# Performance work log

Hardware: AMD Instinct MI355X
Metric: run time of the kernel (lower is better)

Reference implementation:

```python
import jax, jax.numpy as jnp
import numpy as np

B, N, H, D, HS, RS = 4, 512, 16, 64, 1024, 64  # HS = H*D, HSIZE_INSIDE == HSIZE
SCALE = 1.0 / float(np.sqrt(D))


def setup_inputs() -> dict:
    key = jax.random.key(0)
    ks = jax.random.split(key, 11)
    s = 0.02
    return {
        "v": jax.random.normal(ks[0], (B, N, HS), jnp.float32),
        "k": jax.random.normal(ks[1], (B, N, HS), jnp.float32),
        "q": jax.random.normal(ks[2], (B, N, HS), jnp.float32),
        "mask": jax.random.randint(ks[3], (B, 1, N, N), 0, 2).astype(bool),
        "rel_embed": jax.random.uniform(ks[4], (B, N, N, RS), jnp.float32),
        # weights stored as [in, out] (torch Linear applies x @ W.T)
        "Wv": jax.random.normal(ks[5], (HS, HS), jnp.float32) * s,
        "Wk": jax.random.normal(ks[6], (HS, HS), jnp.float32) * s,
        "Wq": jax.random.normal(ks[7], (HS, HS), jnp.float32) * s,
        "Wr": jax.random.normal(ks[8], (RS, H), jnp.float32) * s,
        "br": jax.random.normal(ks[9], (H,), jnp.float32) * s,
        "Wm": jax.random.normal(ks[10], (HS, HS), jnp.float32) * s,
    }


def reference(v, k, q, mask, rel_embed, Wv, Wk, Wq, Wr, br, Wm):
    b, nq, _ = q.shape

    def proj(x, W):  # [b, n, HS] -> [b, H, n, D]
        return (x @ W).reshape(b, -1, H, D).transpose(0, 2, 1, 3)

    vh, kh, qh = proj(v, Wv), proj(k, Wk), proj(q, Wq)
    # learned relative-position bias: relu -> clamp -> log, [b, H, nq, nk]
    r = jax.nn.relu(rel_embed @ Wr + br)
    bias = jnp.log(jnp.clip(r, 1e-6, None)).transpose(0, 3, 1, 2)
    scores = jnp.einsum('bhqd,bhkd->bhqk', qh, kh) * SCALE + bias
    scores = jnp.where(mask, jnp.float32(-1e9), scores)
    att = jax.nn.softmax(scores, axis=-1)  # dropout_r = 0
    atted = jnp.einsum('bhqk,bhkd->bhqd', att, vh)
    atted = atted.transpose(0, 2, 1, 3).reshape(b, nq, H * D)
    return atted @ Wm
```

## Files before the change

### kernel.cpp

```cpp
#include <hip/hip_runtime.h>
#include <hip/hip_bf16.h>


typedef __bf16 bf16_t;
typedef __bf16 bf16x8 __attribute__((ext_vector_type(8)));
typedef float f32x4 __attribute__((ext_vector_type(4)));

__device__ __forceinline__ f32x4 mfma16(bf16x8 a, bf16x8 b, f32x4 c) {
  return __builtin_amdgcn_mfma_f32_16x16x32_bf16(a, b, c, 0, 0, 0);
}
__device__ __forceinline__ f32x4 zero4() {
  f32x4 z; z[0] = 0.f; z[1] = 0.f; z[2] = 0.f; z[3] = 0.f; return z;
}

#define GLOAD_LDS16(gptr, lptr)                                                   \
  __builtin_amdgcn_global_load_lds(                                               \
      (const __attribute__((address_space(1))) unsigned int*)(gptr),              \
      (__attribute__((address_space(3))) unsigned int*)(lptr), 16, 0, 0)

__global__ __launch_bounds__(256) void wtrans_kernel(
    const float* __restrict__ W0, const float* __restrict__ W1,
    const float* __restrict__ W2, const float* __restrict__ W3,
    bf16_t* __restrict__ OutBase,
    const unsigned int* __restrict__ mw, int* __restrict__ flag) {
  const float* W = blockIdx.z == 0 ? W0 : blockIdx.z == 1 ? W1 : blockIdx.z == 2 ? W2 : W3;
  bf16_t* Ot = OutBase + (size_t)blockIdx.z * 1024 * 1024;
  __shared__ float tile[64][68];
  __shared__ int sflag;
  const int tid = threadIdx.x;
  const bool probe = (blockIdx.x == 0 && blockIdx.y == 0 && blockIdx.z == 0);
  if (probe && tid == 0) sflag = 0;
  const int i0 = blockIdx.y * 64, j0 = blockIdx.x * 64;
  const int ri = tid >> 2, rc = (tid & 3) * 16;
  const float* src = W + (size_t)(i0 + ri) * 1024 + j0 + rc;
#pragma unroll
  for (int qq = 0; qq < 4; ++qq) {
    float4 f = *(const float4*)(src + qq * 4);
    *(float4*)(&tile[ri][rc + qq * 4]) = f;
  }
  if (probe) {
    int any = 0;
    for (int i = tid; i < 4096; i += 256) any |= (mw[i] > 1u) ? 1 : 0;
    if (any) atomicOr(&sflag, 1);
  }
  __syncthreads();
  const int wj = tid >> 2, wc = (tid & 3) * 16;
  bf16x8 o0, o1;
#pragma unroll
  for (int s = 0; s < 8; ++s) o0[s] = (bf16_t)tile[wc + s][wj];
#pragma unroll
  for (int s = 0; s < 8; ++s) o1[s] = (bf16_t)tile[wc + 8 + s][wj];
  bf16_t* dst = Ot + (size_t)(j0 + wj) * 1024 + i0 + wc;
  *(bf16x8*)dst = o0;
  *(bf16x8*)(dst + 8) = o1;
  if (probe && tid == 0) *flag = sflag;
}

__global__ __launch_bounds__(256) void cast_qkv(
    const float* __restrict__ q, const float* __restrict__ k, const float* __restrict__ v,
    bf16_t* __restrict__ Qc, bf16_t* __restrict__ Kc, bf16_t* __restrict__ Vc) {
  const size_t gid = (size_t)blockIdx.x * 256 + threadIdx.x;
  const int which = (int)(gid >> 18);
  const size_t off = (gid & 262143) * 8;
  const float* src = which == 0 ? q : which == 1 ? k : v;
  bf16_t* dst = which == 0 ? Qc : which == 1 ? Kc : Vc;
  const float scl = which == 0 ? 0.125f : 1.0f;
  float4 f0 = *(const float4*)(src + off);
  float4 f1 = *(const float4*)(src + off + 4);
  bf16x8 o;
  o[0] = (bf16_t)(f0.x * scl); o[1] = (bf16_t)(f0.y * scl);
  o[2] = (bf16_t)(f0.z * scl); o[3] = (bf16_t)(f0.w * scl);
  o[4] = (bf16_t)(f1.x * scl); o[5] = (bf16_t)(f1.y * scl);
  o[6] = (bf16_t)(f1.z * scl); o[7] = (bf16_t)(f1.w * scl);
  *(bf16x8*)(dst + off) = o;
}

__global__ __launch_bounds__(256) void proj_gemm2(
    const bf16_t* __restrict__ Aq, const bf16_t* __restrict__ Ak, const bf16_t* __restrict__ Av,
    const bf16_t* __restrict__ Bq, const bf16_t* __restrict__ Bk, const bf16_t* __restrict__ Bv,
    bf16_t* __restrict__ Oq, bf16_t* __restrict__ Ok, bf16_t* __restrict__ Ov) {
  const int z = blockIdx.z;
  const bf16_t* A = (z == 0) ? Aq : (z == 1) ? Ak : Av;
  const bf16_t* Bt = (z == 0) ? Bq : (z == 1) ? Bk : Bv;
  bf16_t* Out = (z == 0) ? Oq : (z == 1) ? Ok : Ov;
  __shared__ __align__(16) bf16_t Asm[128 * 64];
  __shared__ __align__(16) bf16_t Bsm[128 * 64];
  const int tid = threadIdx.x, wid = tid >> 6, lane = tid & 63;
  const int lg = lane >> 4, lc = lane & 15;
  const int m0 = blockIdx.y * 128, n0 = blockIdx.x * 128;
  const int wm = (wid >> 1) * 64, wn = (wid & 1) * 64;
  const int sr = lane >> 3;
  const int scch = lane & 7;
  const int srcch = scch ^ sr;
  const bf16_t* Ap[4];
  const bf16_t* Bp[4];
#pragma unroll
  for (int i = 0; i < 4; ++i) {
    const int r = wid * 32 + i * 8 + sr;
    Ap[i] = A + (size_t)(m0 + r) * 1024 + srcch * 8;
    Bp[i] = Bt + (size_t)(n0 + r) * 1024 + srcch * 8;
  }
  f32x4 acc[4][4];
#pragma unroll
  for (int i = 0; i < 4; ++i)
#pragma unroll
    for (int j = 0; j < 4; ++j) acc[i][j] = zero4();

  for (int k0 = 0; k0 < 1024; k0 += 64) {
#pragma unroll
    for (int i = 0; i < 4; ++i) {
      GLOAD_LDS16(Ap[i] + k0, Asm + (wid * 32 + i * 8) * 64);
      GLOAD_LDS16(Bp[i] + k0, Bsm + (wid * 32 + i * 8) * 64);
    }
    __syncthreads();
#pragma unroll
    for (int kk = 0; kk < 2; ++kk) {
      bf16x8 af[4], bfv[4];
#pragma unroll
      for (int i = 0; i < 4; ++i) {
        const int ar = wm + i * 16 + lc;
        af[i] = *(const bf16x8*)(Asm + ar * 64 + ((kk * 4 + lg) ^ (ar & 7)) * 8);
        const int brr = wn + i * 16 + lc;
        bfv[i] = *(const bf16x8*)(Bsm + brr * 64 + ((kk * 4 + lg) ^ (brr & 7)) * 8);
      }
#pragma unroll
      for (int mi = 0; mi < 4; ++mi)
#pragma unroll
        for (int ni = 0; ni < 4; ++ni) acc[mi][ni] = mfma16(af[mi], bfv[ni], acc[mi][ni]);
    }
    __syncthreads();
  }
#pragma unroll
  for (int mi = 0; mi < 4; ++mi)
#pragma unroll
    for (int ni = 0; ni < 4; ++ni)
#pragma unroll
      for (int j = 0; j < 4; ++j) {
        const int m = m0 + wm + mi * 16 + lg * 4 + j;
        const int col = n0 + wn + ni * 16 + lc;
        const int b = m >> 9, n = m & 511;
        const int h = col >> 6, d = col & 63;
        Out[(((size_t)(b * 16 + h)) * 512 + n) * 64 + d] = (bf16_t)acc[mi][ni][j];
      }
}

__global__ __launch_bounds__(256) void bias_kernel(
    const float* __restrict__ rel, const float* __restrict__ Wr,
    const float* __restrict__ br, const void* __restrict__ mask,
    const int* __restrict__ mflag, bf16_t* __restrict__ biasM) {
  const int tid = threadIdx.x, wid = tid >> 6, lane = tid & 63;
  const int lg = lane >> 4, lc = lane & 15;
  const int pair = blockIdx.x;
  const int b = pair >> 9, qrow = pair & 511;
  const int isU8 = *mflag;
  bf16x8 wf[2];
#pragma unroll
  for (int kk = 0; kk < 2; ++kk)
#pragma unroll
    for (int j = 0; j < 8; ++j)
      wf[kk][j] = (bf16_t)Wr[(kk * 32 + lg * 8 + j) * 16 + lc];
  float brv[4];
#pragma unroll
  for (int j = 0; j < 4; ++j) brv[j] = br[lg * 4 + j];
  const float* relrow = rel + (size_t)pair * 512 * 64;
  const size_t mbase = (size_t)b * 512 * 512 + (size_t)qrow * 512;
  bf16_t* outb = biasM + (size_t)b * 16 * 512 * 512 + (size_t)qrow * 512;
#pragma unroll 4
  for (int kt = wid * 8; kt < wid * 8 + 8; ++kt) {
    const int k0 = kt * 16;
    const float* rrow = relrow + (size_t)(k0 + lc) * 64;
    f32x4 acc;
    acc[0] = brv[0]; acc[1] = brv[1]; acc[2] = brv[2]; acc[3] = brv[3];
#pragma unroll
    for (int kk = 0; kk < 2; ++kk) {
      const float4* s = (const float4*)(rrow + kk * 32 + lg * 8);
      float4 f0 = s[0], f1 = s[1];
      bf16x8 bfr;
      bfr[0] = (bf16_t)f0.x; bfr[1] = (bf16_t)f0.y; bfr[2] = (bf16_t)f0.z; bfr[3] = (bf16_t)f0.w;
      bfr[4] = (bf16_t)f1.x; bfr[5] = (bf16_t)f1.y; bfr[6] = (bf16_t)f1.z; bfr[7] = (bf16_t)f1.w;
      acc = mfma16(wf[kk], bfr, acc);
    }
    bool mb;
    if (isU8) mb = ((const unsigned char*)mask)[mbase + k0 + lc] != 0;
    else      mb = ((const int*)mask)[mbase + k0 + lc] != 0;
#pragma unroll
    for (int j = 0; j < 4; ++j) {
      const float valf = mb ? -1e9f : __logf(fmaxf(acc[j], 1e-6f));
      outb[(size_t)(lg * 4 + j) * 512 * 512 + k0 + lc] = (bf16_t)valf;
    }
  }
}

__global__ __launch_bounds__(256) void attn_kernel(
    const bf16_t* __restrict__ Qh, const bf16_t* __restrict__ Kh,
    const bf16_t* __restrict__ Vh, const bf16_t* __restrict__ biasM,
    bf16_t* __restrict__ atted) {
  __shared__ __align__(16) bf16_t Ksm[2][64 * 64];
  __shared__ __align__(16) bf16_t Vtsm[2][64 * 88];
  __shared__ __align__(16) bf16_t Psm[4 * 16 * 64];
  const int tid = threadIdx.x, wid = tid >> 6, lane = tid & 63;
  const int lg = lane >> 4, lc = lane & 15;
  const int bid = blockIdx.x;
  const int qt = bid & 7, h = (bid >> 3) & 15, b = bid >> 7;
  const size_t headoff = (size_t)(b * 16 + h) * 512 * 64;
  const bf16_t* Qb = Qh + headoff;
  const bf16_t* Kb = Kh + headoff;
  const bf16_t* Vb = Vh + headoff;
  const int q0 = qt * 64 + wid * 16;
  const bf16_t* biasb = biasM + ((size_t)(b * 16 + h) * 512 + q0) * 512;

  bf16x8 qf[2];
#pragma unroll
  for (int kk = 0; kk < 2; ++kk)
    qf[kk] = *(const bf16x8*)(Qb + (size_t)(q0 + lc) * 64 + kk * 32 + lg * 8);

  f32x4 Oacc[4];
#pragma unroll
  for (int ds = 0; ds < 4; ++ds) Oacc[ds] = zero4();
  float mrun[4], lrun[4];
#pragma unroll
  for (int j = 0; j < 4; ++j) { mrun[j] = -INFINITY; lrun[j] = 0.f; }

  const int krow = tid & 63, kc0 = (tid >> 6) * 2;
  const int vn = tid & 63, vd0 = (tid >> 6) * 16;
  bf16_t* Pw = Psm + wid * 16 * 64;

#define STAGE(T, BUF)                                                          \
  do {                                                                         \
    const int kb_ = (T) * 64;                                                  \
    _Pragma("unroll") for (int ci = 0; ci < 2; ++ci) {                         \
      const int c_ = kc0 + ci;                                                 \
      bf16x8 kv_ = *(const bf16x8*)(Kb + (size_t)(kb_ + krow) * 64 + c_ * 8);  \
      *(bf16x8*)(Ksm[BUF] + krow * 64 + (c_ ^ (krow & 7)) * 8) = kv_;          \
    }                                                                          \
    bf16x8 v0_ = *(const bf16x8*)(Vb + (size_t)(kb_ + vn) * 64 + vd0);         \
    bf16x8 v1_ = *(const bf16x8*)(Vb + (size_t)(kb_ + vn) * 64 + vd0 + 8);     \
    _Pragma("unroll") for (int i = 0; i < 8; ++i)                              \
        Vtsm[BUF][(vd0 + i) * 88 + vn] = v0_[i];                               \
    _Pragma("unroll") for (int i = 0; i < 8; ++i)                              \
        Vtsm[BUF][(vd0 + 8 + i) * 88 + vn] = v1_[i];                           \
  } while (0)

  STAGE(0, 0);
  __syncthreads();

  for (int t = 0; t < 8; ++t) {
    const int cur = t & 1;
    if (t < 7) STAGE(t + 1, cur ^ 1);

    f32x4 sacc[4];
#pragma unroll
    for (int quad = 0; quad < 4; ++quad)
#pragma unroll
      for (int j = 0; j < 4; ++j)
        sacc[quad][j] = (float)biasb[(size_t)(lg * 4 + j) * 512 + t * 64 + quad * 16 + lc];

    const bf16_t* Kc = Ksm[cur];
#pragma unroll
    for (int quad = 0; quad < 4; ++quad) {
      const int kr = quad * 16 + lc;
#pragma unroll
      for (int kk = 0; kk < 2; ++kk) {
        bf16x8 kf = *(const bf16x8*)(Kc + kr * 64 + ((kk * 4 + lg) ^ (kr & 7)) * 8);
        sacc[quad] = mfma16(qf[kk], kf, sacc[quad]);
      }
    }

    float p[4][4];
#pragma unroll
    for (int j = 0; j < 4; ++j) {
      float tmax = fmaxf(fmaxf(sacc[0][j], sacc[1][j]), fmaxf(sacc[2][j], sacc[3][j]));
#pragma unroll
      for (int mm = 1; mm < 16; mm <<= 1) tmax = fmaxf(tmax, __shfl_xor(tmax, mm));
      const float mnew = fmaxf(mrun[j], tmax);
      const float sf = __expf(mrun[j] - mnew);
      mrun[j] = mnew;
      lrun[j] *= sf;
#pragma unroll
      for (int ds = 0; ds < 4; ++ds) Oacc[ds][j] *= sf;
      float psum = 0.f;
#pragma unroll
      for (int quad = 0; quad < 4; ++quad) {
        const float pv = __expf(sacc[quad][j] - mnew);
        p[quad][j] = pv;
        psum += pv;
      }
      lrun[j] += psum;
    }

#pragma unroll
    for (int quad = 0; quad < 4; ++quad)
#pragma unroll
      for (int j = 0; j < 4; ++j) {
        const int row = lg * 4 + j, col = quad * 16 + lc;
        Pw[row * 64 + ((col >> 3) ^ (row & 7)) * 8 + (col & 7)] = (bf16_t)p[quad][j];
      }

    const bf16_t* Vc = Vtsm[cur];
#pragma unroll
    for (int kk = 0; kk < 2; ++kk) {
      bf16x8 pf = *(const bf16x8*)(Pw + lc * 64 + ((kk * 4 + lg) ^ (lc & 7)) * 8);
#pragma unroll
      for (int ds = 0; ds < 4; ++ds) {
        bf16x8 vf = *(const bf16x8*)(Vc + (ds * 16 + lc) * 88 + kk * 32 + lg * 8);
        Oacc[ds] = mfma16(pf, vf, Oacc[ds]);
      }
    }
    __syncthreads();
  }
#undef STAGE

#pragma unroll
  for (int j = 0; j < 4; ++j) {
    float l = lrun[j];
#pragma unroll
    for (int mm = 1; mm < 16; mm <<= 1) l += __shfl_xor(l, mm);
    lrun[j] = 1.0f / l;
  }
#pragma unroll
  for (int ds = 0; ds < 4; ++ds)
#pragma unroll
    for (int j = 0; j < 4; ++j) {
      const int n = q0 + lg * 4 + j;
      const int d = ds * 16 + lc;
      atted[((size_t)b * 512 + n) * 1024 + h * 64 + d] = (bf16_t)(Oacc[ds][j] * lrun[j]);
    }
}

__global__ __launch_bounds__(256) void out_gemm2(
    const bf16_t* __restrict__ A, const bf16_t* __restrict__ Bt, float* __restrict__ Out) {
  __shared__ __align__(16) bf16_t Asm[128 * 64];
  __shared__ __align__(16) bf16_t Bsm[128 * 64];
  const int tid = threadIdx.x, wid = tid >> 6, lane = tid & 63;
  const int lg = lane >> 4, lc = lane & 15;
  const int m0 = blockIdx.y * 128, n0 = blockIdx.x * 128;
  const int wm = (wid >> 1) * 64, wn = (wid & 1) * 64;
  const int sr = lane >> 3, scch = lane & 7;
  const int srcch = scch ^ sr;
  const bf16_t* Ap[4];
  const bf16_t* Bp[4];
#pragma unroll
  for (int i = 0; i < 4; ++i) {
    const int r = wid * 32 + i * 8 + sr;
    Ap[i] = A + (size_t)(m0 + r) * 1024 + srcch * 8;
    Bp[i] = Bt + (size_t)(n0 + r) * 1024 + srcch * 8;
  }
  f32x4 acc[4][4];
#pragma unroll
  for (int i = 0; i < 4; ++i)
#pragma unroll
    for (int j = 0; j < 4; ++j) acc[i][j] = zero4();

  for (int k0 = 0; k0 < 1024; k0 += 64) {
#pragma unroll
    for (int i = 0; i < 4; ++i) {
      GLOAD_LDS16(Ap[i] + k0, Asm + (wid * 32 + i * 8) * 64);
      GLOAD_LDS16(Bp[i] + k0, Bsm + (wid * 32 + i * 8) * 64);
    }
    __syncthreads();
#pragma unroll
    for (int kk = 0; kk < 2; ++kk) {
      bf16x8 af[4], bfv[4];
#pragma unroll
      for (int i = 0; i < 4; ++i) {
        const int ar = wm + i * 16 + lc;
        af[i] = *(const bf16x8*)(Asm + ar * 64 + ((kk * 4 + lg) ^ (ar & 7)) * 8);
        const int brr = wn + i * 16 + lc;
        bfv[i] = *(const bf16x8*)(Bsm + brr * 64 + ((kk * 4 + lg) ^ (brr & 7)) * 8);
      }
#pragma unroll
      for (int mi = 0; mi < 4; ++mi)
#pragma unroll
        for (int ni = 0; ni < 4; ++ni) acc[mi][ni] = mfma16(af[mi], bfv[ni], acc[mi][ni]);
    }
    __syncthreads();
  }
#pragma unroll
  for (int mi = 0; mi < 4; ++mi)
#pragma unroll
    for (int ni = 0; ni < 4; ++ni)
#pragma unroll
      for (int j = 0; j < 4; ++j) {
        const int m = m0 + wm + mi * 16 + lg * 4 + j;
        const int col = n0 + wn + ni * 16 + lc;
        Out[(size_t)m * 1024 + col] = acc[mi][ni][j];
      }
}

extern "C" void kernel_launch(void* const* d_in, const int* in_sizes, int n_in,
                              void* d_out, int out_size, void* d_ws, size_t ws_size,
                              hipStream_t stream) {
  const float* v = (const float*)d_in[0];
  const float* k = (const float*)d_in[1];
  const float* q = (const float*)d_in[2];
  const void* mask = d_in[3];
  const float* rel = (const float*)d_in[4];
  const float* Wv = (const float*)d_in[5];
  const float* Wk = (const float*)d_in[6];
  const float* Wq = (const float*)d_in[7];
  const float* Wr = (const float*)d_in[8];
  const float* br = (const float*)d_in[9];
  const float* Wm = (const float*)d_in[10];

  char* ws = (char*)d_ws;
  bf16_t* Wt = (bf16_t*)ws;
  bf16_t* Qh = (bf16_t*)(ws + ((size_t)8 << 20));
  bf16_t* Kh = (bf16_t*)(ws + ((size_t)12 << 20));
  bf16_t* Vh = (bf16_t*)(ws + ((size_t)16 << 20));
  bf16_t* biasM = (bf16_t*)(ws + ((size_t)20 << 20));
  bf16_t* atted = (bf16_t*)(ws + ((size_t)52 << 20));
  bf16_t* Qc = (bf16_t*)(ws + ((size_t)56 << 20));
  bf16_t* Kc = (bf16_t*)(ws + ((size_t)60 << 20));
  bf16_t* Vc = (bf16_t*)(ws + ((size_t)64 << 20));
  int* mflag = (int*)(ws + ((size_t)68 << 20));
  bf16_t* Wvt = Wt + 0 * 1048576;
  bf16_t* Wkt = Wt + 1 * 1048576;
  bf16_t* Wqt = Wt + 2 * 1048576;
  bf16_t* Wmt = Wt + 3 * 1048576;

  wtrans_kernel<<<dim3(16, 16, 4), 256, 0, stream>>>(Wv, Wk, Wq, Wm, Wt,
                                                     (const unsigned int*)mask, mflag);
  cast_qkv<<<dim3(3072), 256, 0, stream>>>(q, k, v, Qc, Kc, Vc);
  proj_gemm2<<<dim3(8, 16, 3), 256, 0, stream>>>(Qc, Kc, Vc, Wqt, Wkt, Wvt, Qh, Kh, Vh);
  bias_kernel<<<dim3(2048), 256, 0, stream>>>(rel, Wr, br, mask, mflag, biasM);
  attn_kernel<<<dim3(512), 256, 0, stream>>>(Qh, Kh, Vh, biasM, atted);
  out_gemm2<<<dim3(8, 16), 256, 0, stream>>>(atted, Wmt, (float*)d_out);
}
```

Baseline: 160.6 us.

## Merge weight transpose with QKV cast, and bias with projection GEMM, into two launches

Combines the weight-transpose and QKV-cast kernels into one launch that branches on block index, and combines the relative-position bias kernel with the QKV projection GEMM into a single 'fat' launch. This cuts launch overhead and lets the memory-bound bias work run alongside the compute-bound GEMM blocks on the GPU. The fused kernel carries the GEMM's shared-memory allocation even for bias blocks, which may reduce occupancy for those blocks.

```diff
diff --git a/kernel.cpp b/kernel.cpp
--- a/kernel.cpp
+++ b/kernel.cpp
@@ -18,19 +18,39 @@
       (const __attribute__((address_space(1))) unsigned int*)(gptr),              \
       (__attribute__((address_space(3))) unsigned int*)(lptr), 16, 0, 0)
 
-__global__ __launch_bounds__(256) void wtrans_kernel(
+__global__ __launch_bounds__(256) void prep_kernel(
     const float* __restrict__ W0, const float* __restrict__ W1,
     const float* __restrict__ W2, const float* __restrict__ W3,
     bf16_t* __restrict__ OutBase,
+    const float* __restrict__ q, const float* __restrict__ k, const float* __restrict__ v,
+    bf16_t* __restrict__ Qc, bf16_t* __restrict__ Kc, bf16_t* __restrict__ Vc,
     const unsigned int* __restrict__ mw, int* __restrict__ flag) {
-  const float* W = blockIdx.z == 0 ? W0 : blockIdx.z == 1 ? W1 : blockIdx.z == 2 ? W2 : W3;
-  bf16_t* Ot = OutBase + (size_t)blockIdx.z * 1024 * 1024;
+  const int tid = threadIdx.x;
+  if (blockIdx.x >= 1024) {
+    const size_t gid = (size_t)(blockIdx.x - 1024) * 256 + tid;
+    const int which = (int)(gid >> 18);
+    const size_t off = (gid & 262143) * 8;
+    const float* src = which == 0 ? q : which == 1 ? k : v;
+    bf16_t* dst = which == 0 ? Qc : which == 1 ? Kc : Vc;
+    const float scl = which == 0 ? 0.125f : 1.0f;
+    float4 f0 = *(const float4*)(src + off);
+    float4 f1 = *(const float4*)(src + off + 4);
+    bf16x8 o;
+    o[0] = (bf16_t)(f0.x * scl); o[1] = (bf16_t)(f0.y * scl);
+    o[2] = (bf16_t)(f0.z * scl); o[3] = (bf16_t)(f0.w * scl);
+    o[4] = (bf16_t)(f1.x * scl); o[5] = (bf16_t)(f1.y * scl);
+    o[6] = (bf16_t)(f1.z * scl); o[7] = (bf16_t)(f1.w * scl);
+    *(bf16x8*)(dst + off) = o;
+    return;
+  }
+  const int wz = blockIdx.x >> 8, wy = (blockIdx.x >> 4) & 15, wx = blockIdx.x & 15;
+  const float* W = wz == 0 ? W0 : wz == 1 ? W1 : wz == 2 ? W2 : W3;
+  bf16_t* Ot = OutBase + (size_t)wz * 1024 * 1024;
   __shared__ float tile[64][68];
   __shared__ int sflag;
-  const int tid = threadIdx.x;
-  const bool probe = (blockIdx.x == 0 && blockIdx.y == 0 && blockIdx.z == 0);
+  const bool probe = (blockIdx.x == 0);
   if (probe && tid == 0) sflag = 0;
-  const int i0 = blockIdx.y * 64, j0 = blockIdx.x * 64;
+  const int i0 = wy * 64, j0 = wx * 64;
   const int ri = tid >> 2, rc = (tid & 3) * 16;
   const float* src = W + (size_t)(i0 + ri) * 1024 + j0 + rc;
 #pragma unroll
@@ -56,38 +76,68 @@
   if (probe && tid == 0) *flag = sflag;
 }
 
-__global__ __launch_bounds__(256) void cast_qkv(
-    const float* __restrict__ q, const float* __restrict__ k, const float* __restrict__ v,
-    bf16_t* __restrict__ Qc, bf16_t* __restrict__ Kc, bf16_t* __restrict__ Vc) {
-  const size_t gid = (size_t)blockIdx.x * 256 + threadIdx.x;
-  const int which = (int)(gid >> 18);
-  const size_t off = (gid & 262143) * 8;
-  const float* src = which == 0 ? q : which == 1 ? k : v;
-  bf16_t* dst = which == 0 ? Qc : which == 1 ? Kc : Vc;
-  const float scl = which == 0 ? 0.125f : 1.0f;
-  float4 f0 = *(const float4*)(src + off);
-  float4 f1 = *(const float4*)(src + off + 4);
-  bf16x8 o;
-  o[0] = (bf16_t)(f0.x * scl); o[1] = (bf16_t)(f0.y * scl);
-  o[2] = (bf16_t)(f0.z * scl); o[3] = (bf16_t)(f0.w * scl);
-  o[4] = (bf16_t)(f1.x * scl); o[5] = (bf16_t)(f1.y * scl);
-  o[6] = (bf16_t)(f1.z * scl); o[7] = (bf16_t)(f1.w * scl);
-  *(bf16x8*)(dst + off) = o;
-}
-
-__global__ __launch_bounds__(256) void proj_gemm2(
+__global__ __launch_bounds__(256) void fat_kernel(
+    const float* __restrict__ rel, const float* __restrict__ Wr,
+    const float* __restrict__ br, const void* __restrict__ mask,
+    const int* __restrict__ mflag, bf16_t* __restrict__ biasM,
     const bf16_t* __restrict__ Aq, const bf16_t* __restrict__ Ak, const bf16_t* __restrict__ Av,
     const bf16_t* __restrict__ Bq, const bf16_t* __restrict__ Bk, const bf16_t* __restrict__ Bv,
     bf16_t* __restrict__ Oq, bf16_t* __restrict__ Ok, bf16_t* __restrict__ Ov) {
-  const int z = blockIdx.z;
-  const bf16_t* A = (z == 0) ? Aq : (z == 1) ? Ak : Av;
-  const bf16_t* Bt = (z == 0) ? Bq : (z == 1) ? Bk : Bv;
-  bf16_t* Out = (z == 0) ? Oq : (z == 1) ? Ok : Ov;
   __shared__ __align__(16) bf16_t Asm[128 * 64];
   __shared__ __align__(16) bf16_t Bsm[128 * 64];
   const int tid = threadIdx.x, wid = tid >> 6, lane = tid & 63;
   const int lg = lane >> 4, lc = lane & 15;
-  const int m0 = blockIdx.y * 128, n0 = blockIdx.x * 128;
+
+  if (blockIdx.x < 2048) {
+    const int pair = blockIdx.x;
+    const int b = pair >> 9, qrow = pair & 511;
+    const int isU8 = *mflag;
+    bf16x8 wf[2];
+#pragma unroll
+    for (int kk = 0; kk < 2; ++kk)
+#pragma unroll
+      for (int j = 0; j < 8; ++j)
+        wf[kk][j] = (bf16_t)Wr[(kk * 32 + lg * 8 + j) * 16 + lc];
+    float brv[4];
+#pragma unroll
+    for (int j = 0; j < 4; ++j) brv[j] = br[lg * 4 + j];
+    const float* relrow = rel + (size_t)pair * 512 * 64;
+    const size_t mbase = (size_t)b * 512 * 512 + (size_t)qrow * 512;
+    bf16_t* outb = biasM + (size_t)b * 16 * 512 * 512 + (size_t)qrow * 512;
+#pragma unroll 4
+    for (int kt = wid * 8; kt < wid * 8 + 8; ++kt) {
+      const int k0 = kt * 16;
+      const float* rrow = relrow + (size_t)(k0 + lc) * 64;
+      f32x4 acc;
+      acc[0] = brv[0]; acc[1] = brv[1]; acc[2] = brv[2]; acc[3] = brv[3];
+#pragma unroll
+      for (int kk = 0; kk < 2; ++kk) {
+        const float4* s = (const float4*)(rrow + kk * 32 + lg * 8);
+        float4 f0 = s[0], f1 = s[1];
+        bf16x8 bfr;
+        bfr[0] = (bf16_t)f0.x; bfr[1] = (bf16_t)f0.y; bfr[2] = (bf16_t)f0.z; bfr[3] = (bf16_t)f0.w;
+        bfr[4] = (bf16_t)f1.x; bfr[5] = (bf16_t)f1.y; bfr[6] = (bf16_t)f1.z; bfr[7] = (bf16_t)f1.w;
+        acc = mfma16(wf[kk], bfr, acc);
+      }
+      bool mb;
+      if (isU8) mb = ((const unsigned char*)mask)[mbase + k0 + lc] != 0;
+      else      mb = ((const int*)mask)[mbase + k0 + lc] != 0;
+#pragma unroll
+      for (int j = 0; j < 4; ++j) {
+        const float valf = mb ? -1e9f : __logf(fmaxf(acc[j], 1e-6f));
+        outb[(size_t)(lg * 4 + j) * 512 * 512 + k0 + lc] = (bf16_t)valf;
+      }
+    }
+    return;
+  }
+
+  const int idx = blockIdx.x - 2048;
+  const int z = idx >> 7, rem = idx & 127;
+  const int byy = rem >> 3, bxx = rem & 7;
+  const bf16_t* A = (z == 0) ? Aq : (z == 1) ? Ak : Av;
+  const bf16_t* Bt = (z == 0) ? Bq : (z == 1) ? Bk : Bv;
+  bf16_t* Out = (z == 0) ? Oq : (z == 1) ? Ok : Ov;
+  const int m0 = byy * 128, n0 = bxx * 128;
   const int wm = (wid >> 1) * 64, wn = (wid & 1) * 64;
   const int sr = lane >> 3;
   const int scch = lane & 7;
@@ -142,53 +192,6 @@
         const int h = col >> 6, d = col & 63;
         Out[(((size_t)(b * 16 + h)) * 512 + n) * 64 + d] = (bf16_t)acc[mi][ni][j];
       }
-}
-
-__global__ __launch_bounds__(256) void bias_kernel(
-    const float* __restrict__ rel, const float* __restrict__ Wr,
-    const float* __restrict__ br, const void* __restrict__ mask,
-    const int* __restrict__ mflag, bf16_t* __restrict__ biasM) {
-  const int tid = threadIdx.x, wid = tid >> 6, lane = tid & 63;
-  const int lg = lane >> 4, lc = lane & 15;
-  const int pair = blockIdx.x;
-  const int b = pair >> 9, qrow = pair & 511;
-  const int isU8 = *mflag;
-  bf16x8 wf[2];
-#pragma unroll
-  for (int kk = 0; kk < 2; ++kk)
-#pragma unroll
-    for (int j = 0; j < 8; ++j)
-      wf[kk][j] = (bf16_t)Wr[(kk * 32 + lg * 8 + j) * 16 + lc];
-  float brv[4];
-#pragma unroll
-  for (int j = 0; j < 4; ++j) brv[j] = br[lg * 4 + j];
-  const float* relrow = rel + (size_t)pair * 512 * 64;
-  const size_t mbase = (size_t)b * 512 * 512 + (size_t)qrow * 512;
-  bf16_t* outb = biasM + (size_t)b * 16 * 512 * 512 + (size_t)qrow * 512;
-#pragma unroll 4
-  for (int kt = wid * 8; kt < wid * 8 + 8; ++kt) {
-    const int k0 = kt * 16;
-    const float* rrow = relrow + (size_t)(k0 + lc) * 64;
-    f32x4 acc;
-    acc[0] = brv[0]; acc[1] = brv[1]; acc[2] = brv[2]; acc[3] = brv[3];
-#pragma unroll
-    for (int kk = 0; kk < 2; ++kk) {
-      const float4* s = (const float4*)(rrow + kk * 32 + lg * 8);
-      float4 f0 = s[0], f1 = s[1];
-      bf16x8 bfr;
-      bfr[0] = (bf16_t)f0.x; bfr[1] = (bf16_t)f0.y; bfr[2] = (bf16_t)f0.z; bfr[3] = (bf16_t)f0.w;
-      bfr[4] = (bf16_t)f1.x; bfr[5] = (bf16_t)f1.y; bfr[6] = (bf16_t)f1.z; bfr[7] = (bf16_t)f1.w;
-      acc = mfma16(wf[kk], bfr, acc);
-    }
-    bool mb;
-    if (isU8) mb = ((const unsigned char*)mask)[mbase + k0 + lc] != 0;
-    else      mb = ((const int*)mask)[mbase + k0 + lc] != 0;
-#pragma unroll
-    for (int j = 0; j < 4; ++j) {
-      const float valf = mb ? -1e9f : __logf(fmaxf(acc[j], 1e-6f));
-      outb[(size_t)(lg * 4 + j) * 512 * 512 + k0 + lc] = (bf16_t)valf;
-    }
-  }
 }
 
 __global__ __launch_bounds__(256) void attn_kernel(
@@ -418,11 +421,10 @@
   bf16_t* Wqt = Wt + 2 * 1048576;
   bf16_t* Wmt = Wt + 3 * 1048576;
 
-  wtrans_kernel<<<dim3(16, 16, 4), 256, 0, stream>>>(Wv, Wk, Wq, Wm, Wt,
-                                                     (const unsigned int*)mask, mflag);
-  cast_qkv<<<dim3(3072), 256, 0, stream>>>(q, k, v, Qc, Kc, Vc);
-  proj_gemm2<<<dim3(8, 16, 3), 256, 0, stream>>>(Qc, Kc, Vc, Wqt, Wkt, Wvt, Qh, Kh, Vh);
-  bias_kernel<<<dim3(2048), 256, 0, stream>>>(rel, Wr, br, mask, mflag, biasM);
+  prep_kernel<<<dim3(4096), 256, 0, stream>>>(Wv, Wk, Wq, Wm, Wt, q, k, v, Qc, Kc, Vc,
+                                              (const unsigned int*)mask, mflag);
+  fat_kernel<<<dim3(2432), 256, 0, stream>>>(rel, Wr, br, mask, mflag, biasM,
+                                             Qc, Kc, Vc, Wqt, Wkt, Wvt, Qh, Kh, Vh);
   attn_kernel<<<dim3(512), 256, 0, stream>>>(Qh, Kh, Vh, biasM, atted);
   out_gemm2<<<dim3(8, 16), 256, 0, stream>>>(atted, Wmt, (float*)d_out);
 }
```

Result: faster. 144.8 us (-9.9%).
